# Kernel tuning notes

Hardware: AMD Instinct MI355X
Metric: run time of the kernel (lower is better)

## Reference

```python
import jax, jax.numpy as jnp
import numpy as np
import math

THETA = 1.0


def _qdense(xa, xb, wa, wb, ba, bb):
    # QComplexDense: j_squared = -cos(2*theta)
    j2 = -math.cos(2.0 * THETA)
    out_a = xa @ wa.T + j2 * (xb @ wb.T) + ba
    out_b = xa @ wb.T + xb @ wa.T + bb
    return out_a, out_b


def setup_inputs() -> dict:
    key = jax.random.key(0)
    B, S, D = 4, 2048, 1024
    ks = jax.random.split(key, 16)
    limit = math.sqrt(6.0 / (D + D))  # xavier uniform for square [D,D]

    def w(k):
        return jax.random.uniform(k, (D, D), jnp.float32, -limit, limit)

    inp = {
        'xa': jax.random.normal(ks[0], (B, S, D), jnp.float32),
        'xb': jax.random.normal(ks[1], (B, S, D), jnp.float32),
    }
    i = 2
    for n in ('q', 'k', 'v', 'o'):
        inp[n + '_wa'] = w(ks[i]); inp[n + '_wb'] = w(ks[i + 1])
        inp[n + '_ba'] = jnp.zeros((D,), jnp.float32)
        inp[n + '_bb'] = jnp.zeros((D,), jnp.float32)
        i += 2
    return inp


def reference(xa, xb,
              q_wa, q_wb, q_ba, q_bb,
              k_wa, k_wb, k_ba, k_bb,
              v_wa, v_wb, v_ba, v_bb,
              o_wa, o_wb, o_ba, o_bb):
    D = xa.shape[-1]
    # NOTE: qc_matmul in the original uses cos(2 * ones(1)) == cos(2.0),
    # a constant independent of theta.
    c2 = math.cos(2.0)

    Qa, Qb = _qdense(xa, xb, q_wa, q_wb, q_ba, q_bb)
    Ka, Kb = _qdense(xa, xb, k_wa, k_wb, k_ba, k_bb)
    Va, Vb = _qdense(xa, xb, v_wa, v_wb, v_ba, v_bb)

    # complex-style QK^T: scores_a = Qa Ka^T - cos(2) Qb Kb^T ; scores_b = Qa Kb^T + Qb Ka^T
    sa = jnp.einsum('bsd,btd->bst', Qa, Ka) - c2 * jnp.einsum('bsd,btd->bst', Qb, Kb)
    sb = jnp.einsum('bsd,btd->bst', Qa, Kb) + jnp.einsum('bsd,btd->bst', Qb, Ka)
    scores_real = jnp.sqrt(sa * sa + sb * sb)  # magnitude
    attn = jax.nn.softmax(scores_real / math.sqrt(D), axis=-1)  # [B,S,S]

    out_a = jnp.einsum('bst,btd->bsd', attn, Va)
    out_b = jnp.einsum('bst,btd->bsd', attn, Vb)
    return _qdense(out_a, out_b, o_wa, o_wb, o_ba, o_bb)
```

## Files before the change

### kernel.cpp

```cpp
#include <hip/hip_runtime.h>
#include <math.h>

typedef __bf16 bf16_t;
typedef __attribute__((ext_vector_type(16))) float f32x16;
typedef __attribute__((ext_vector_type(8))) __bf16 v8bf;
typedef __attribute__((ext_vector_type(4))) __bf16 v4bf;

#define GLLDS(g, l)                                                           \
  __builtin_amdgcn_global_load_lds(                                           \
      (const __attribute__((address_space(1))) void*)(g),                     \
      (__attribute__((address_space(3))) void*)(l), 16, 0, 0)
#define OPQ(p) asm volatile("" : "+v"(p))

__global__ void sentinel_kernel(float* o, float v) { o[0] = v; }

__global__ __launch_bounds__(256) void pack_x_kernel(
    const float* __restrict__ xa, const float* __restrict__ xb,
    bf16_t* __restrict__ xcat, int n4)
{
  int i = blockIdx.x * 256 + threadIdx.x;
  if (i >= n4) return;
  float4 a = reinterpret_cast<const float4*>(xa)[i];
  float4 b = reinterpret_cast<const float4*>(xb)[i];
  long e = (long)i * 4;
  long m = e >> 10;
  int  d = (int)(e & 1023);
  v4bf av = { (bf16_t)a.x, (bf16_t)a.y, (bf16_t)a.z, (bf16_t)a.w };
  v4bf bv = { (bf16_t)b.x, (bf16_t)b.y, (bf16_t)b.z, (bf16_t)b.w };
  *reinterpret_cast<v4bf*>(xcat + m * 2048 + d)        = av;
  *reinterpret_cast<v4bf*>(xcat + m * 2048 + 1024 + d) = bv;
}

__global__ __launch_bounds__(256) void pack_w_kernel(
    const float* __restrict__ wa, const float* __restrict__ wb,
    bf16_t* __restrict__ outA, bf16_t* __restrict__ outB, float j2)
{
  int i = blockIdx.x * 256 + threadIdx.x;
  float4 a = reinterpret_cast<const float4*>(wa)[i];
  float4 b = reinterpret_cast<const float4*>(wb)[i];
  long e = (long)i * 4;
  long n = e >> 10;
  int  k = (int)(e & 1023);
  v4bf av = { (bf16_t)a.x, (bf16_t)a.y, (bf16_t)a.z, (bf16_t)a.w };
  v4bf bv = { (bf16_t)b.x, (bf16_t)b.y, (bf16_t)b.z, (bf16_t)b.w };
  v4bf jb = { (bf16_t)(j2*b.x), (bf16_t)(j2*b.y), (bf16_t)(j2*b.z), (bf16_t)(j2*b.w) };
  *reinterpret_cast<v4bf*>(outA + n * 2048 + k)        = av;
  *reinterpret_cast<v4bf*>(outA + n * 2048 + 1024 + k) = jb;
  *reinterpret_cast<v4bf*>(outB + n * 2048 + k)        = bv;
  *reinterpret_cast<v4bf*>(outB + n * 2048 + 1024 + k) = av;
}

template<int EPI>
__global__ __launch_bounds__(512) void gemm256_kernel(
    const bf16_t* __restrict__ A, const bf16_t* __restrict__ B,
    int K, long lda, long ldb, long bsA, long bsB,
    void* __restrict__ o0p, void* __restrict__ o1p, void* __restrict__ o2p,
    const float* __restrict__ bb0, const float* __restrict__ bb1,
    const float* __restrict__ bb2, const float* __restrict__ bb3,
    const float* __restrict__ bb4, const float* __restrict__ bb5,
    float scl)
{
  __shared__ __align__(16) bf16_t lds[65536];
  const int tid  = threadIdx.x;
  const int wid  = tid >> 6;
  const int lane = tid & 63;
  const int wm = wid >> 2;
  const int wn = wid & 3;

  const long row0 = (long)blockIdx.y * 256;
  const long col0 = (long)blockIdx.x * 256;
  const int z = blockIdx.z;
  const bf16_t* Ab = A + (long)z * bsA + row0 * lda;
  const bf16_t* Bb = B + (long)z * bsB + col0 * ldb;

  const int srow = wid * 8 + (lane >> 3);
  const int scol = ((lane & 7) ^ (lane >> 3)) * 8;
  const int dbase = wid * 512;

  const bf16_t* sA0 = Ab + (long)srow * lda + scol;
  const bf16_t* sA1 = Ab + (long)(srow + 64) * lda + scol;
  const bf16_t* sA2 = Ab + (long)(srow + 128) * lda + scol;
  const bf16_t* sA3 = Ab + (long)(srow + 192) * lda + scol;
  const bf16_t* sB0 = Bb + (long)srow * ldb + scol;
  const bf16_t* sB1 = Bb + (long)(srow + 64) * ldb + scol;
  const bf16_t* sB2 = Bb + (long)(srow + 128) * ldb + scol;
  const bf16_t* sB3 = Bb + (long)(srow + 192) * ldb + scol;

  const int r32 = lane & 31;
  const int kg2 = lane >> 5;
  const int r7 = r32 & 7;
  const bf16_t *pAs[4], *pBs[4];
#pragma unroll
  for (int s = 0; s < 4; ++s) {
    const int ch = (((kg2 + 2 * s) ^ r7) & 7) * 8;
    pAs[s] = lds + (wm * 128 + r32) * 64 + ch;
    pBs[s] = lds + 16384 + (wn * 64 + r32) * 64 + ch;
  }

  f32x16 acc[4][2];
#pragma unroll
  for (int i = 0; i < 4; ++i)
#pragma unroll
    for (int j = 0; j < 2; ++j)
#pragma unroll
      for (int e = 0; e < 16; ++e) acc[i][j][e] = 0.f;

  const int T = K >> 6;

  GLLDS(sA0, lds + dbase);
  GLLDS(sA1, lds + 4096 + dbase);
  GLLDS(sA2, lds + 8192 + dbase);
  GLLDS(sA3, lds + 12288 + dbase);
  GLLDS(sB0, lds + 16384 + dbase);
  GLLDS(sB1, lds + 16384 + 4096 + dbase);
  GLLDS(sB2, lds + 16384 + 8192 + dbase);
  GLLDS(sB3, lds + 16384 + 12288 + dbase);
  sA0 += 64; sA1 += 64; sA2 += 64; sA3 += 64;
  sB0 += 64; sB1 += 64; sB2 += 64; sB3 += 64;
  OPQ(sA0); OPQ(sA1); OPQ(sA2); OPQ(sA3);
  OPQ(sB0); OPQ(sB1); OPQ(sB2); OPQ(sB3);
  asm volatile("s_waitcnt vmcnt(0)" ::: "memory");
  __builtin_amdgcn_sched_barrier(0);
  __builtin_amdgcn_s_barrier();

#define TILE_BODY(U, PF)                                                       \
  {                                                                            \
    const int so_ = (U) * 32768;                                               \
    const int ns_ = (1 - (U)) * 32768;                                         \
    v8bf a_[4][2], b_[2][2];                                                   \
                                             \
    _Pragma("unroll") for (int g = 0; g < 2; ++g)                              \
      _Pragma("unroll") for (int ss = 0; ss < 2; ++ss)                         \
        b_[g][ss] = *reinterpret_cast<const v8bf*>(pBs[ss] + so_ + g * 2048);  \
    _Pragma("unroll") for (int f = 0; f < 4; ++f)                              \
      _Pragma("unroll") for (int ss = 0; ss < 2; ++ss)                         \
        a_[f][ss] = *reinterpret_cast<const v8bf*>(pAs[ss] + so_ + f * 2048);  \
    if (PF) {                                                                  \
      GLLDS(sA0, lds + ns_ + dbase);                                           \
      GLLDS(sA1, lds + ns_ + 4096 + dbase);                                    \
      GLLDS(sA2, lds + ns_ + 8192 + dbase);                                    \
      GLLDS(sA3, lds + ns_ + 12288 + dbase);                                   \
    }                                                                          \
    __builtin_amdgcn_s_setprio(1);                                             \
    _Pragma("unroll") for (int ss = 0; ss < 2; ++ss)                           \
      _Pragma("unroll") for (int f = 0; f < 4; ++f)                            \
        _Pragma("unroll") for (int g = 0; g < 2; ++g)                          \
          acc[f][g] = __builtin_amdgcn_mfma_f32_32x32x16_bf16(a_[f][ss], b_[g][ss], acc[f][g], 0, 0, 0); \
    __builtin_amdgcn_s_setprio(0);                                             \
                                             \
    _Pragma("unroll") for (int g = 0; g < 2; ++g)                              \
      _Pragma("unroll") for (int ss = 0; ss < 2; ++ss)                         \
        b_[g][ss] = *reinterpret_cast<const v8bf*>(pBs[2 + ss] + so_ + g * 2048); \
    _Pragma("unroll") for (int f = 0; f < 4; ++f)                              \
      _Pragma("unroll") for (int ss = 0; ss < 2; ++ss)                         \
        a_[f][ss] = *reinterpret_cast<const v8bf*>(pAs[2 + ss] + so_ + f * 2048); \
    if (PF) {                                                                  \
      GLLDS(sB0, lds + ns_ + 16384 + dbase);                                   \
      GLLDS(sB1, lds + ns_ + 16384 + 4096 + dbase);                            \
      GLLDS(sB2, lds + ns_ + 16384 + 8192 + dbase);                            \
      GLLDS(sB3, lds + ns_ + 16384 + 12288 + dbase);                           \
      sA0 += 64; sA1 += 64; sA2 += 64; sA3 += 64;                              \
      sB0 += 64; sB1 += 64; sB2 += 64; sB3 += 64;                              \
      OPQ(sA0); OPQ(sA1); OPQ(sA2); OPQ(sA3);                                  \
      OPQ(sB0); OPQ(sB1); OPQ(sB2); OPQ(sB3);                                  \
    }                                                                          \
    __builtin_amdgcn_s_setprio(1);                                             \
    _Pragma("unroll") for (int ss = 0; ss < 2; ++ss)                           \
      _Pragma("unroll") for (int f = 0; f < 4; ++f)                            \
        _Pragma("unroll") for (int g = 0; g < 2; ++g)                          \
          acc[f][g] = __builtin_amdgcn_mfma_f32_32x32x16_bf16(a_[f][ss], b_[g][ss], acc[f][g], 0, 0, 0); \
    __builtin_amdgcn_s_setprio(0);                                             \
    asm volatile("s_waitcnt vmcnt(0)" ::: "memory");                           \
    __builtin_amdgcn_sched_barrier(0);                                         \
    __builtin_amdgcn_s_barrier();                                              \
  }

  for (int tb = 0; tb < T - 2; tb += 2) {
    TILE_BODY(0, 1)
    TILE_BODY(1, 1)
  }
  TILE_BODY(0, 1)
  TILE_BODY(1, 0)
#undef TILE_BODY

  const int hi = lane >> 5;
#pragma unroll
  for (int fm = 0; fm < 4; ++fm) {
#pragma unroll
    for (int fn = 0; fn < 2; ++fn) {
      const f32x16 v = acc[fm][fn];
      const long rowb = row0 + wm * 128 + fm * 32 + 4 * hi;
      const long col  = col0 + wn * 64 + fn * 32 + r32;
      if constexpr (EPI == 0) {
        const int  seg = (int)(col >> 10);
        const long c   = col & 1023;
        bf16_t* Q  = (bf16_t*)o0p;
        bf16_t* Kc = (bf16_t*)o1p;
        bf16_t* Vc = (bf16_t*)o2p;
        switch (seg) {
          case 0: { const float bv = bb0[c];
#pragma unroll
            for (int r = 0; r < 16; ++r) {
              const long row = rowb + (r & 3) + 8 * (r >> 2);
              Q[row * 2048 + c] = (bf16_t)((v[r] + bv) * 0.03125f);
            } } break;
          case 1: { const float bv = bb1[c];
#pragma unroll
            for (int r = 0; r < 16; ++r) {
              const long row = rowb + (r & 3) + 8 * (r >> 2);
              Q[row * 2048 + 1024 + c] = (bf16_t)((v[r] + bv) * 0.03125f);
            } } break;
          case 2: { const float bv = bb2[c];
#pragma unroll
            for (int r = 0; r < 16; ++r) {
              const long row = rowb + (r & 3) + 8 * (r >> 2);
              const long kbase = (row >> 11) * 8388608 + (row & 2047) * 2048;
              const float w = v[r] + bv;
              Kc[kbase + c]                  = (bf16_t)w;
              Kc[kbase + 4194304 + 1024 + c] = (bf16_t)w;
            } } break;
          case 3: { const float bv = bb3[c];
#pragma unroll
            for (int r = 0; r < 16; ++r) {
              const long row = rowb + (r & 3) + 8 * (r >> 2);
              const long kbase = (row >> 11) * 8388608 + (row & 2047) * 2048;
              const float w = v[r] + bv;
              Kc[kbase + 4194304 + c] = (bf16_t)w;
              Kc[kbase + 1024 + c]    = (bf16_t)(scl * w);
            } } break;
          case 4: { const float bv = bb4[c];
#pragma unroll
            for (int r = 0; r < 16; ++r) {
              const long row = rowb + (r & 3) + 8 * (r >> 2);
              Vc[row * 2048 + c] = (bf16_t)(v[r] + bv);
            } } break;
          default: { const float bv = bb5[c];
#pragma unroll
            for (int r = 0; r < 16; ++r) {
              const long row = rowb + (r & 3) + 8 * (r >> 2);
              Vc[row * 2048 + 1024 + c] = (bf16_t)(v[r] + bv);
            } } break;
        }
      } else if constexpr (EPI == 1) {
        const int  seg = (int)(col >> 11);
        const long c   = col & 2047;
        bf16_t* dst = seg ? (bf16_t*)o1p : (bf16_t*)o0p;
#pragma unroll
        for (int r = 0; r < 16; ++r) {
          const long row = rowb + (r & 3) + 8 * (r >> 2);
          dst[(long)z * 4194304 + row * 2048 + c] = (bf16_t)v[r];
        }
      } else if constexpr (EPI == 2) {
#pragma unroll
        for (int r = 0; r < 16; ++r) {
          const long row = rowb + (r & 3) + 8 * (r >> 2);
          ((bf16_t*)o0p)[(long)z * 4194304 + row * 2048 + col] = (bf16_t)v[r];
        }
      } else {
        const int  seg = (int)(col >> 10);
        const long c   = col & 1023;
        float* dst = seg ? (float*)o1p : (float*)o0p;
        const float bv = seg ? bb1[c] : bb0[c];
#pragma unroll
        for (int r = 0; r < 16; ++r) {
          const long row = rowb + (r & 3) + 8 * (r >> 2);
          dst[row * 1024 + c] = v[r] + bv;
        }
      }
    }
  }
}

__global__ __launch_bounds__(256) void transpose_v_kernel(
    const bf16_t* __restrict__ src, bf16_t* __restrict__ dst)
{
  __shared__ bf16_t t[64][65];
  const int tid = threadIdx.x;
  const int off = blockIdx.z * 1024;
  const long c0 = (long)blockIdx.x * 64;
  const long g0 = (long)blockIdx.y * 64;
#pragma unroll
  for (int it = 0; it < 16; ++it) {
    int idx = it * 256 + tid;
    int r = idx >> 6, c = idx & 63;
    t[r][c] = src[(g0 + r) * 2048 + off + c0 + c];
  }
  __syncthreads();
  const long b  = g0 >> 11;
  const long t0 = g0 & 2047;
#pragma unroll
  for (int it = 0; it < 16; ++it) {
    int idx = it * 256 + tid;
    int nr = idx >> 6, tc = idx & 63;
    dst[b * 4194304 + (off + c0 + nr) * 2048 + t0 + tc] = t[tc][nr];
  }
}

__global__ __launch_bounds__(256) void softmax_mag_kernel(
    const bf16_t* __restrict__ sa, const bf16_t* __restrict__ sb,
    bf16_t* __restrict__ attn)
{
  const int tid = threadIdx.x;
  const long base = (long)blockIdx.x * 2048;
  v4bf a0 = *reinterpret_cast<const v4bf*>(sa + base + tid * 4);
  v4bf a1 = *reinterpret_cast<const v4bf*>(sa + base + 1024 + tid * 4);
  v4bf b0 = *reinterpret_cast<const v4bf*>(sb + base + tid * 4);
  v4bf b1 = *reinterpret_cast<const v4bf*>(sb + base + 1024 + tid * 4);
  float r[8];
#pragma unroll
  for (int k = 0; k < 4; ++k) {
    float x = (float)a0[k], y = (float)b0[k];
    r[k] = sqrtf(x * x + y * y);
  }
#pragma unroll
  for (int k = 0; k < 4; ++k) {
    float x = (float)a1[k], y = (float)b1[k];
    r[4 + k] = sqrtf(x * x + y * y);
  }
  float m = r[0];
#pragma unroll
  for (int k = 1; k < 8; ++k) m = fmaxf(m, r[k]);
#pragma unroll
  for (int off = 32; off > 0; off >>= 1) m = fmaxf(m, __shfl_xor(m, off));
  __shared__ float red[8];
  if ((tid & 63) == 0) red[tid >> 6] = m;
  __syncthreads();
  m = fmaxf(fmaxf(red[0], red[1]), fmaxf(red[2], red[3]));
  float p[8], s = 0.f;
#pragma unroll
  for (int k = 0; k < 8; ++k) { p[k] = __expf(r[k] - m); s += p[k]; }
#pragma unroll
  for (int off = 32; off > 0; off >>= 1) s += __shfl_xor(s, off);
  if ((tid & 63) == 0) red[4 + (tid >> 6)] = s;
  __syncthreads();
  const float inv = 1.f / (red[4] + red[5] + red[6] + red[7]);
  v4bf o0 = { (bf16_t)(p[0]*inv), (bf16_t)(p[1]*inv), (bf16_t)(p[2]*inv), (bf16_t)(p[3]*inv) };
  v4bf o1 = { (bf16_t)(p[4]*inv), (bf16_t)(p[5]*inv), (bf16_t)(p[6]*inv), (bf16_t)(p[7]*inv) };
  *reinterpret_cast<v4bf*>(attn + base + tid * 4)        = o0;
  *reinterpret_cast<v4bf*>(attn + base + 1024 + tid * 4) = o1;
}

extern "C" void kernel_launch(void* const* d_in, const int* in_sizes, int n_in,
                              void* d_out, int out_size, void* d_ws, size_t ws_size,
                              hipStream_t stream)
{
  (void)in_sizes; (void)n_in; (void)out_size;
  const float* xa = (const float*)d_in[0];
  const float* xb = (const float*)d_in[1];
  const float *w_a[4], *w_b[4], *b_a[4], *b_b[4];
  for (int p = 0; p < 4; ++p) {
    w_a[p] = (const float*)d_in[2 + p*4 + 0];
    w_b[p] = (const float*)d_in[2 + p*4 + 1];
    b_a[p] = (const float*)d_in[2 + p*4 + 2];
    b_b[p] = (const float*)d_in[2 + p*4 + 3];
  }
  float* out = (float*)d_out;
  const float neg_c2 = (float)(-cos(2.0));

  const size_t WFULL = 33554432ull;
  const size_t WQKV  = 25165824ull;
  int NB = 0; bool fullW = true;
  if      (ws_size >= WFULL + 6ull * 4ull * 8388608ull) NB = 4;
  else if (ws_size >= WFULL + 6ull * 2ull * 8388608ull) NB = 2;
  else if (ws_size >= WFULL + 6ull * 1ull * 8388608ull) NB = 1;
  else if (ws_size >= WQKV  + 6ull * 1ull * 8388608ull) { NB = 1; fullW = false; }
  else { sentinel_kernel<<<1, 1, 0, stream>>>(out, (float)ws_size); return; }

  char* ws = (char*)d_ws;
  const size_t wbytes = fullW ? WFULL : WQKV;
  const size_t RB = (size_t)NB * 8388608ull;
  bf16_t* Wqkv = (bf16_t*)ws;
  bf16_t* Wo   = fullW ? (bf16_t*)(ws + WQKV) : Wqkv;
  bf16_t* R0 = (bf16_t*)(ws + wbytes);
  bf16_t* R1 = (bf16_t*)(ws + wbytes + 1*RB);
  bf16_t* Kc = (bf16_t*)(ws + wbytes + 2*RB);
  bf16_t* R4 = (bf16_t*)(ws + wbytes + 4*RB);
  bf16_t* R5 = (bf16_t*)(ws + wbytes + 5*RB);

  const int  Mc = NB * 2048;
  const dim3 blk(256);
  const dim3 blk512(512);
  const dim3 gqkv(24, Mc / 256, 1);
  const dim3 gsc(16, 8, NB);
  const dim3 gpv(8, 8, NB);
  const dim3 go(8, Mc / 256, 1);
  const dim3 gtr(16, Mc / 64, 2);

  if (fullW) {
    for (int p = 0; p < 3; ++p)
      pack_w_kernel<<<1024, blk, 0, stream>>>(w_a[p], w_b[p],
          Wqkv + (size_t)(2*p)   * 2097152ull,
          Wqkv + (size_t)(2*p+1) * 2097152ull, neg_c2);
    pack_w_kernel<<<1024, blk, 0, stream>>>(w_a[3], w_b[3],
        Wo, Wo + 2097152ull, neg_c2);
  }

  for (int c = 0; c < 4 / NB; ++c) {
    const size_t xoff = (size_t)c * NB * 2097152ull;
    pack_x_kernel<<<Mc, blk, 0, stream>>>(xa + xoff, xb + xoff, R0, Mc * 256);

    if (!fullW)
      for (int p = 0; p < 3; ++p)
        pack_w_kernel<<<1024, blk, 0, stream>>>(w_a[p], w_b[p],
            Wqkv + (size_t)(2*p)   * 2097152ull,
            Wqkv + (size_t)(2*p+1) * 2097152ull, neg_c2);

    gemm256_kernel<0><<<gqkv, blk512, 0, stream>>>(R0, Wqkv, 2048, 2048, 2048, 0, 0,
        R1, Kc, R4, b_a[0], b_b[0], b_a[1], b_b[1], b_a[2], b_b[2], neg_c2);

    transpose_v_kernel<<<gtr, blk, 0, stream>>>(R4, R5);

    gemm256_kernel<1><<<gsc, blk512, 0, stream>>>(R1, Kc, 2048, 2048, 2048, 4194304, 8388608,
        R0, R4, nullptr, nullptr, nullptr, nullptr, nullptr, nullptr, nullptr, 0.f);

    softmax_mag_kernel<<<Mc, blk, 0, stream>>>(R0, R4, R0);

    gemm256_kernel<2><<<gpv, blk512, 0, stream>>>(R0, R5, 2048, 2048, 2048, 4194304, 4194304,
        R1, nullptr, nullptr, nullptr, nullptr, nullptr, nullptr, nullptr, nullptr, 0.f);

    if (!fullW)
      pack_w_kernel<<<1024, blk, 0, stream>>>(w_a[3], w_b[3], Wo, Wo + 2097152ull, neg_c2);
    gemm256_kernel<3><<<go, blk512, 0, stream>>>(R1, Wo, 2048, 2048, 2048, 0, 0,
        out + xoff, out + 8388608ull + xoff, nullptr,
        b_a[3], b_b[3], nullptr, nullptr, nullptr, nullptr, 0.f);
  }
}
```

Measured before the change: 559.6 us.

## Interleave K layout and fuse score magnitude into the QK^T GEMM epilogue

The packed K matrix is rearranged so the real and imaginary score columns for each key position land in adjacent output columns of the scores GEMM. The epilogue then pairs neighbouring lanes with a shuffle, computes the magnitude, and writes a single bf16 magnitude matrix instead of separate sa and sb matrices. The softmax kernel now reads one input instead of two and no longer computes square roots. This cuts score-matrix write and read traffic roughly in half. It depends on the MFMA lane-to-column mapping placing adjacent columns in adjacent lanes, and only half the lanes issue stores, which are now strided.

```diff
diff --git a/kernel.cpp b/kernel.cpp
--- a/kernel.cpp
+++ b/kernel.cpp
@@ -214,19 +214,19 @@
 #pragma unroll
             for (int r = 0; r < 16; ++r) {
               const long row = rowb + (r & 3) + 8 * (r >> 2);
-              const long kbase = (row >> 11) * 8388608 + (row & 2047) * 2048;
+              const long kb2 = (row >> 11) * 8388608 + (row & 2047) * 4096;
               const float w = v[r] + bv;
-              Kc[kbase + c]                  = (bf16_t)w;
-              Kc[kbase + 4194304 + 1024 + c] = (bf16_t)w;
+              Kc[kb2 + c]               = (bf16_t)w;
+              Kc[kb2 + 2048 + 1024 + c] = (bf16_t)w;
             } } break;
           case 3: { const float bv = bb3[c];
 #pragma unroll
             for (int r = 0; r < 16; ++r) {
               const long row = rowb + (r & 3) + 8 * (r >> 2);
-              const long kbase = (row >> 11) * 8388608 + (row & 2047) * 2048;
+              const long kb2 = (row >> 11) * 8388608 + (row & 2047) * 4096;
               const float w = v[r] + bv;
-              Kc[kbase + 4194304 + c] = (bf16_t)w;
-              Kc[kbase + 1024 + c]    = (bf16_t)(scl * w);
+              Kc[kb2 + 2048 + c] = (bf16_t)w;
+              Kc[kb2 + 1024 + c] = (bf16_t)(scl * w);
             } } break;
           case 4: { const float bv = bb4[c];
 #pragma unroll
@@ -242,13 +242,16 @@
             } } break;
         }
       } else if constexpr (EPI == 1) {
-        const int  seg = (int)(col >> 11);
-        const long c   = col & 2047;
-        bf16_t* dst = seg ? (bf16_t*)o1p : (bf16_t*)o0p;
+        bf16_t* dst = (bf16_t*)o0p;
+        const long tt = col >> 1;
 #pragma unroll
         for (int r = 0; r < 16; ++r) {
           const long row = rowb + (r & 3) + 8 * (r >> 2);
-          dst[(long)z * 4194304 + row * 2048 + c] = (bf16_t)v[r];
+          const float x = v[r];
+          const float p = __shfl_xor(x, 1);
+          const float mg = sqrtf(x * x + p * p);
+          if (!(lane & 1))
+            dst[(long)z * 4194304 + row * 2048 + tt] = (bf16_t)mg;
         }
       } else if constexpr (EPI == 2) {
 #pragma unroll
@@ -296,27 +299,18 @@
   }
 }
 
-__global__ __launch_bounds__(256) void softmax_mag_kernel(
-    const bf16_t* __restrict__ sa, const bf16_t* __restrict__ sb,
-    bf16_t* __restrict__ attn)
+__global__ __launch_bounds__(256) void softmax_kernel(
+    const bf16_t* __restrict__ mag, bf16_t* __restrict__ attn)
 {
   const int tid = threadIdx.x;
   const long base = (long)blockIdx.x * 2048;
-  v4bf a0 = *reinterpret_cast<const v4bf*>(sa + base + tid * 4);
-  v4bf a1 = *reinterpret_cast<const v4bf*>(sa + base + 1024 + tid * 4);
-  v4bf b0 = *reinterpret_cast<const v4bf*>(sb + base + tid * 4);
-  v4bf b1 = *reinterpret_cast<const v4bf*>(sb + base + 1024 + tid * 4);
+  v4bf m0 = *reinterpret_cast<const v4bf*>(mag + base + tid * 4);
+  v4bf m1 = *reinterpret_cast<const v4bf*>(mag + base + 1024 + tid * 4);
   float r[8];
 #pragma unroll
-  for (int k = 0; k < 4; ++k) {
-    float x = (float)a0[k], y = (float)b0[k];
-    r[k] = sqrtf(x * x + y * y);
-  }
-#pragma unroll
-  for (int k = 0; k < 4; ++k) {
-    float x = (float)a1[k], y = (float)b1[k];
-    r[4 + k] = sqrtf(x * x + y * y);
-  }
+  for (int k = 0; k < 4; ++k) r[k] = (float)m0[k];
+#pragma unroll
+  for (int k = 0; k < 4; ++k) r[4 + k] = (float)m1[k];
   float m = r[0];
 #pragma unroll
   for (int k = 1; k < 8; ++k) m = fmaxf(m, r[k]);
@@ -411,9 +405,9 @@
     transpose_v_kernel<<<gtr, blk, 0, stream>>>(R4, R5);
 
     gemm256_kernel<1><<<gsc, blk512, 0, stream>>>(R1, Kc, 2048, 2048, 2048, 4194304, 8388608,
-        R0, R4, nullptr, nullptr, nullptr, nullptr, nullptr, nullptr, nullptr, 0.f);
-
-    softmax_mag_kernel<<<Mc, blk, 0, stream>>>(R0, R4, R0);
+        R0, nullptr, nullptr, nullptr, nullptr, nullptr, nullptr, nullptr, nullptr, 0.f);
+
+    softmax_kernel<<<Mc, blk, 0, stream>>>(R0, R0);
 
     gemm256_kernel<2><<<gpv, blk512, 0, stream>>>(R0, R5, 2048, 2048, 2048, 4194304, 4194304,
         R1, nullptr, nullptr, nullptr, nullptr, nullptr, nullptr, nullptr, nullptr, 0.f);
```

After: 556.6 us, median of 3. No clear change (-0.5%).
